# Kernel optimization log

Measured on AMD Instinct MI355X. Metric: run time of the kernel, lower is better.

Reference implementation:

```python
import jax, jax.numpy as jnp
import numpy as np

EPS = 1e-8
SCALE_FACTOR = 5.0
ITERS = 3

def _ln(x, g, b):
    m = x.mean(-1, keepdims=True)
    v = ((x - m) ** 2).mean(-1, keepdims=True)
    return (x - m) / jnp.sqrt(v + 1e-5) * g + b

def setup_inputs() -> dict:
    key = jax.random.key(0)
    ks = jax.random.split(key, 12)
    B, N, K, D = 8, 1024, 8, 256
    n01 = lambda k, s, sc=0.02: jax.random.normal(k, s, jnp.float32) * sc
    return {
        "inputs": jax.random.normal(ks[0], (B, N, D), jnp.float32),
        "conditioning": jax.random.normal(ks[1], (B, K, D + 4), jnp.float32),
        "ni_g": jnp.ones((D,), jnp.float32), "ni_b": jnp.zeros((D,), jnp.float32),
        "ns_g": jnp.ones((D,), jnp.float32), "ns_b": jnp.zeros((D,), jnp.float32),
        "wq": n01(ks[2], (D, D)), "wk": n01(ks[3], (D, D)), "wv": n01(ks[4], (D, D)),
        "gp_w": n01(ks[5], (2, D), 0.5), "gp_b": jnp.zeros((D,), jnp.float32),
        "ge_ln_g": jnp.ones((D,), jnp.float32), "ge_ln_b": jnp.zeros((D,), jnp.float32),
        "ge_w1": n01(ks[6], (D, 2 * D)), "ge_b1": jnp.zeros((2 * D,), jnp.float32),
        "ge_w2": n01(ks[7], (2 * D, D)), "ge_b2": jnp.zeros((D,), jnp.float32),
        "gru_wih": n01(ks[8], (3 * D, D)), "gru_whh": n01(ks[9], (3 * D, D)),
        "gru_bih": jnp.zeros((3 * D,), jnp.float32), "gru_bhh": jnp.zeros((3 * D,), jnp.float32),
    }

def _forward(inputs, conditioning, ni_g, ni_b, ns_g, ns_b, wq, wk, wv,
             gp_w, gp_b, ge_ln_g, ge_ln_b, ge_w1, ge_b1, ge_w2, ge_b2,
             gru_wih, gru_whh, gru_bih, gru_bhh):
    B, N, FD = inputs.shape
    D = wq.shape[1]
    attn_scale = D ** -0.5
    side = int(round(N ** 0.5))
    xs = jnp.linspace(-1.0, 1.0, side)
    abs_grid = jnp.stack(jnp.meshgrid(xs, xs, indexing="ij"), -1).reshape(N, 2)  # (N,2)

    x = _ln(inputs, ni_g, ni_b)
    k = x @ wk  # (B,N,D)
    v = x @ wv  # (B,N,D)

    def grid_enc(t):
        h = _ln(t, ge_ln_g, ge_ln_b)
        h = jax.nn.relu(h @ ge_w1 + ge_b1)
        return h @ ge_w2 + ge_b2

    def step(slots_full, update):
        slots = slots_full[..., :-4]                       # (B,K,D)
        pos = jnp.clip(slots_full[..., -4:-2], -1.0, 1.0)  # (B,K,2)
        scl = jnp.clip(slots_full[..., -2:], 1e-3, 2.0)    # (B,K,2)
        rel_grid = (abs_grid[None, None] - pos[:, :, None]) / (scl[:, :, None] * SCALE_FACTOR)  # (B,K,N,2)
        rel_enc = rel_grid @ gp_w + gp_b                   # (B,K,N,D)
        rel_k = grid_enc(k[:, None] + rel_enc)             # (B,K,N,D)
        rel_v = grid_enc(v[:, None] + rel_enc)             # (B,K,N,D)
        q = _ln(slots, ns_g, ns_b) @ wq                    # (B,K,D)
        dots = jnp.einsum("bkd,bknd->bkn", q, rel_k) * attn_scale
        attn0 = jax.nn.softmax(dots, axis=1)               # softmax over the SLOT axis
        attn = attn0 + EPS
        attn = attn / attn.sum(-1, keepdims=True)
        pos_n = jnp.einsum("bkn,nd->bkd", attn0, abs_grid)
        spread = (abs_grid[None, None] - pos_n[:, :, None]) ** 2  # (B,K,N,2)
        scl_n = jnp.clip(jnp.sqrt(jnp.einsum("bkn,bknd->bkd", attn0 + EPS, spread)), 1e-3, 2.0)
        if update:
            upd = jnp.einsum("bknd,bkn->bkd", rel_v, attn)
            gx = upd @ gru_wih.T + gru_bih
            gh = slots @ gru_whh.T + gru_bhh
            xr, xz, xn = jnp.split(gx, 3, -1)
            hr, hz, hn = jnp.split(gh, 3, -1)
            r = jax.nn.sigmoid(xr + hr)
            z = jax.nn.sigmoid(xz + hz)
            n_ = jnp.tanh(xn + r * hn)
            slots = (1.0 - z) * n_ + z * slots
        return jnp.concatenate([slots, pos_n, scl_n], -1), attn0, rel_grid

    attn0 = rel_grid = None
    for i in range(ITERS + 1):
        conditioning, attn0, rel_grid = step(conditioning, i < ITERS)
    return conditioning, attn0, rel_grid

def reference(inputs, conditioning, ni_g, ni_b, ns_g, ns_b, wq, wk, wv,
              gp_w, gp_b, ge_ln_g, ge_ln_b, ge_w1, ge_b1, ge_w2, ge_b2,
              gru_wih, gru_whh, gru_bih, gru_bhh):
    return _forward(inputs, conditioning, ni_g, ni_b, ns_g, ns_b, wq, wk, wv,
                    gp_w, gp_b, ge_ln_g, ge_ln_b, ge_w1, ge_b1, ge_w2, ge_b2,
                    gru_wih, gru_whh, gru_bih, gru_bhh)
```

## Files before the change

kernel.cpp:

```cpp
#include <hip/hip_runtime.h>
#include <math.h>

#define NB 8
#define NN 1024
#define NK 8
#define ND 256
#define ND2 512
#define NBK 64
#define EPSA 1e-8f
#define LNEPS 1e-5f
#define GSTEP (2.0f/31.0f)

using short8 = __attribute__((ext_vector_type(8))) short;
using short4v = __attribute__((ext_vector_type(4))) short;
using floatx4 = __attribute__((ext_vector_type(4))) float;

__device__ __forceinline__ short f2bf(float f) {
  unsigned u = __builtin_bit_cast(unsigned, f);
  u += 0x7fffu + ((u >> 16) & 1u);
  return (short)(u >> 16);
}
__device__ __forceinline__ float bf2f(short s) {
  unsigned u = ((unsigned)(unsigned short)s) << 16;
  return __builtin_bit_cast(float, u);
}

__global__ __launch_bounds__(256) void k_cvt_all(
    const float* __restrict__ w1, const float* __restrict__ w2,
    const float* __restrict__ wk, const float* __restrict__ wv,
    const float* __restrict__ wih, const float* __restrict__ whh,
    const float* __restrict__ wq, const float* __restrict__ b2,
    short* __restrict__ w1T, short* __restrict__ wkT, short* __restrict__ wvT,
    short* __restrict__ whhB, short* __restrict__ w2B,
    float* __restrict__ bx, float* __restrict__ vb) {
  const int idx = blockIdx.x * 256 + threadIdx.x;
  if (idx < 131072) {
    const int n = idx >> 8, k = idx & 255;
    const int dst = ((n >> 4) * 8 + (k >> 5)) * 512 + ((k >> 3) & 3) * 128 + (n & 15) * 8 + (k & 7);
    w1T[dst] = f2bf(w1[(size_t)k * 512 + n]);
  } else if (idx < 196608) {
    const int i = idx - 131072;
    const int n = i >> 8, k = i & 255;
    const int dst = ((n >> 4) * 8 + (k >> 5)) * 512 + ((k >> 3) & 3) * 128 + (n & 15) * 8 + (k & 7);
    wkT[dst] = f2bf(wk[(size_t)k * 256 + n]);
  } else if (idx < 262144) {
    const int i = idx - 196608;
    const int n = i >> 8, k = i & 255;
    const int dst = ((n >> 4) * 8 + (k >> 5)) * 512 + ((k >> 3) & 3) * 128 + (n & 15) * 8 + (k & 7);
    wvT[dst] = f2bf(wv[(size_t)k * 256 + n]);
  } else if (idx < 458752) {
    const int i = idx - 262144;
    whhB[i] = f2bf(whh[i]);
  } else if (idx < 589824) {
    const int i = idx - 458752;
    w2B[i] = f2bf(w2[i]);
  } else if (idx < 590592) {
    const int j = idx - 589824;
    float s = 0.f;
#pragma unroll 8
    for (int d = 0; d < 256; d++) s = fmaf(b2[d], wih[(size_t)j * 256 + d], s);
    bx[j] = s;
  } else if (idx < 590848) {
    const int e = idx - 590592;
    float s = 0.f;
#pragma unroll 8
    for (int d = 0; d < 256; d++) s = fmaf(wq[(size_t)e * 256 + d], b2[d], s);
    vb[e] = s;
  }
}

__global__ __launch_bounds__(256, 2) void k_mm(
    const float* __restrict__ wih, const float* __restrict__ wq,
    const short* __restrict__ w2B,
    short* __restrict__ WXT, short* __restrict__ MQ) {
  const int z = blockIdx.z;
  if (z == 1 && blockIdx.x >= 4) return;
  const float* __restrict__ A = z ? wq : wih;
  short* __restrict__ C = z ? MQ : WXT;
  __shared__ __align__(16) short As[64 * 264];
  const int row0 = blockIdx.x * 64;
  const int col0 = blockIdx.y * 128;
  const int t = threadIdx.x;
  const int wave = t >> 6, lane = t & 63, l15 = lane & 15, quad = lane >> 4;
  {
    const int r = t >> 2, sub = t & 3;
    const float* ar = A + (size_t)(row0 + r) * 256;
#pragma unroll
    for (int ii = 0; ii < 16; ii++) {
      const int d = sub * 4 + ii * 16;
      const float4 v = *(const float4*)(ar + d);
      short4v pk = {f2bf(v.x), f2bf(v.y), f2bf(v.z), f2bf(v.w)};
      *(short4v*)&As[r * 264 + d] = pk;
    }
  }
  __syncthreads();
  const short* wp = w2B + (size_t)(col0 + wave * 32 + l15) * 256 + quad * 8;
  floatx4 acc[4][2];
#pragma unroll
  for (int mt = 0; mt < 4; mt++)
#pragma unroll
    for (int nt = 0; nt < 2; nt++) acc[mt][nt] = (floatx4){0.f, 0.f, 0.f, 0.f};
#pragma unroll
  for (int kk = 0; kk < 8; kk++) {
    short8 af[4];
#pragma unroll
    for (int mt = 0; mt < 4; mt++)
      af[mt] = *(const short8*)&As[(mt * 16 + l15) * 264 + kk * 32 + quad * 8];
    short8 bf[2];
#pragma unroll
    for (int nt = 0; nt < 2; nt++)
      bf[nt] = *(const short8*)(wp + nt * 16 * 256 + kk * 32);
#pragma unroll
    for (int mt = 0; mt < 4; mt++)
#pragma unroll
      for (int nt = 0; nt < 2; nt++)
        acc[mt][nt] = __builtin_amdgcn_mfma_f32_16x16x32_bf16(af[mt], bf[nt], acc[mt][nt], 0, 0, 0);
  }
#pragma unroll
  for (int mt = 0; mt < 4; mt++)
#pragma unroll
    for (int nt = 0; nt < 2; nt++)
#pragma unroll
      for (int j = 0; j < 4; j++)
        C[(size_t)(row0 + mt * 16 + quad * 4 + j) * 512 + col0 + wave * 32 + nt * 16 + l15] =
            f2bf(acc[mt][nt][j]);
}

__global__ __launch_bounds__(256, 2) void k_gemm_kv_mfma(
    const float* __restrict__ inp,
    const float* __restrict__ nig, const float* __restrict__ nib,
    const short* __restrict__ wkT, const short* __restrict__ wvT,
    float* __restrict__ kout, float* __restrict__ vout) {
  __shared__ __align__(16) short tln[64 * 264];
  const short* __restrict__ WT = blockIdx.z ? wvT : wkT;
  float* __restrict__ out = blockIdx.z ? vout : kout;
  const int row0 = blockIdx.x * 64;
  const int t = threadIdx.x;
  const int wave = t >> 6, lane = t & 63, l15 = lane & 15, quad = lane >> 4;
  {
    const int r = t >> 2, sub = t & 3;
    const float* xr = inp + (size_t)(row0 + r) * ND;
    float tv[64];
    float sum = 0.f, ssq = 0.f;
#pragma unroll
    for (int ii = 0; ii < 16; ii++) {
      const int d = sub * 4 + ii * 16;
      const float4 xv = *(const float4*)(xr + d);
      tv[ii * 4 + 0] = xv.x; sum += xv.x; ssq += xv.x * xv.x;
      tv[ii * 4 + 1] = xv.y; sum += xv.y; ssq += xv.y * xv.y;
      tv[ii * 4 + 2] = xv.z; sum += xv.z; ssq += xv.z * xv.z;
      tv[ii * 4 + 3] = xv.w; sum += xv.w; ssq += xv.w * xv.w;
    }
    sum += __shfl_xor(sum, 1); ssq += __shfl_xor(ssq, 1);
    sum += __shfl_xor(sum, 2); ssq += __shfl_xor(ssq, 2);
    const float mean = sum * (1.0f / ND);
    const float var = ssq * (1.0f / ND) - mean * mean;
    const float rstd = rsqrtf(var + LNEPS);
#pragma unroll
    for (int ii = 0; ii < 16; ii++) {
      const int d = sub * 4 + ii * 16;
      const float4 gg = *(const float4*)(nig + d);
      const float4 bb = *(const float4*)(nib + d);
      short4v pk;
      pk.x = f2bf((tv[ii * 4 + 0] - mean) * rstd * gg.x + bb.x);
      pk.y = f2bf((tv[ii * 4 + 1] - mean) * rstd * gg.y + bb.y);
      pk.z = f2bf((tv[ii * 4 + 2] - mean) * rstd * gg.z + bb.z);
      pk.w = f2bf((tv[ii * 4 + 3] - mean) * rstd * gg.w + bb.w);
      *(short4v*)&tln[r * 264 + d] = pk;
    }
  }
  __syncthreads();
  floatx4 acc[4][4];
#pragma unroll
  for (int mt = 0; mt < 4; mt++)
#pragma unroll
    for (int nt = 0; nt < 4; nt++) acc[mt][nt] = (floatx4){0.f, 0.f, 0.f, 0.f};
  const short* wp = WT + (size_t)(wave * 32) * 512 + (size_t)lane * 8;
#pragma unroll
  for (int kk = 0; kk < 8; kk++) {
    short8 af[4];
#pragma unroll
    for (int mt = 0; mt < 4; mt++)
      af[mt] = *(const short8*)&tln[(mt * 16 + l15) * 264 + kk * 32 + quad * 8];
    short8 bf[4];
#pragma unroll
    for (int nt = 0; nt < 4; nt++)
      bf[nt] = *(const short8*)(wp + (nt * 8 + kk) * 512);
#pragma unroll
    for (int mt = 0; mt < 4; mt++)
#pragma unroll
      for (int nt = 0; nt < 4; nt++)
        acc[mt][nt] = __builtin_amdgcn_mfma_f32_16x16x32_bf16(af[mt], bf[nt], acc[mt][nt], 0, 0, 0);
  }
#pragma unroll
  for (int mt = 0; mt < 4; mt++)
#pragma unroll
    for (int nt = 0; nt < 4; nt++)
#pragma unroll
      for (int j = 0; j < 4; j++)
        out[(size_t)(row0 + mt * 16 + quad * 4 + j) * ND + wave * 64 + nt * 16 + l15] = acc[mt][nt][j];
}

__global__ __launch_bounds__(256, 2) void k_kw(
    const float* __restrict__ kbuf, const float* __restrict__ vbuf,
    const float* __restrict__ gpb, const float* __restrict__ gpw,
    const float* __restrict__ lng,
    const short* __restrict__ w1T,
    short* __restrict__ KWk, short* __restrict__ KWv,
    float* __restrict__ momk, float* __restrict__ momv) {
  __shared__ __align__(16) short tln[64 * 264];
  const float* __restrict__ src = blockIdx.z ? vbuf : kbuf;
  short* __restrict__ KW = blockIdx.z ? KWv : KWk;
  float* __restrict__ mom = blockIdx.z ? momv : momk;
  const int row0 = blockIdx.x * 64;
  const int t = threadIdx.x;
  const int wave = t >> 6, lane = t & 63, l15 = lane & 15, quad = lane >> 4;
  {
    const int r = t >> 2, sub = t & 3;
    const float* xr = src + (size_t)(row0 + r) * ND;
    float su = 0.f, sq = 0.f, sa = 0.f, sb = 0.f;
#pragma unroll
    for (int ii = 0; ii < 16; ii++) {
      const int d = sub * 4 + ii * 16;
      const float4 xv = *(const float4*)(xr + d);
      const float4 pb = *(const float4*)(gpb + d);
      const float4 wa = *(const float4*)(gpw + d);
      const float4 wb = *(const float4*)(gpw + ND + d);
      const float4 gg = *(const float4*)(lng + d);
      const float u0 = xv.x + pb.x, u1 = xv.y + pb.y, u2 = xv.z + pb.z, u3 = xv.w + pb.w;
      su += u0 + u1 + u2 + u3;
      sq += u0 * u0 + u1 * u1 + u2 * u2 + u3 * u3;
      sa += u0 * wa.x + u1 * wa.y + u2 * wa.z + u3 * wa.w;
      sb += u0 * wb.x + u1 * wb.y + u2 * wb.z + u3 * wb.w;
      short4v pk = {f2bf(u0 * gg.x), f2bf(u1 * gg.y), f2bf(u2 * gg.z), f2bf(u3 * gg.w)};
      *(short4v*)&tln[r * 264 + d] = pk;
    }
    su += __shfl_xor(su, 1); sq += __shfl_xor(sq, 1);
    sa += __shfl_xor(sa, 1); sb += __shfl_xor(sb, 1);
    su += __shfl_xor(su, 2); sq += __shfl_xor(sq, 2);
    sa += __shfl_xor(sa, 2); sb += __shfl_xor(sb, 2);
    if (sub == 0) {
      mom[(size_t)(row0 + r) * 4 + 0] = su * (1.0f / ND);
      mom[(size_t)(row0 + r) * 4 + 1] = sq * (1.0f / ND);
      mom[(size_t)(row0 + r) * 4 + 2] = sa * (1.0f / ND);
      mom[(size_t)(row0 + r) * 4 + 3] = sb * (1.0f / ND);
    }
  }
  __syncthreads();
  floatx4 acc[4][8];
#pragma unroll
  for (int mt = 0; mt < 4; mt++)
#pragma unroll
    for (int nt = 0; nt < 8; nt++) acc[mt][nt] = (floatx4){0.f, 0.f, 0.f, 0.f};
  const short* w1p = w1T + (size_t)(wave * 64) * 512 + (size_t)lane * 8;
#pragma unroll
  for (int kk = 0; kk < 8; kk++) {
    short8 af[4];
#pragma unroll
    for (int mt = 0; mt < 4; mt++)
      af[mt] = *(const short8*)&tln[(mt * 16 + l15) * 264 + kk * 32 + quad * 8];
    short8 bf[8];
#pragma unroll
    for (int nt = 0; nt < 8; nt++)
      bf[nt] = *(const short8*)(w1p + (nt * 8 + kk) * 512);
#pragma unroll
    for (int mt = 0; mt < 4; mt++)
#pragma unroll
      for (int nt = 0; nt < 8; nt++)
        acc[mt][nt] = __builtin_amdgcn_mfma_f32_16x16x32_bf16(af[mt], bf[nt], acc[mt][nt], 0, 0, 0);
  }
#pragma unroll
  for (int mt = 0; mt < 4; mt++)
#pragma unroll
    for (int nt = 0; nt < 8; nt++)
#pragma unroll
      for (int j = 0; j < 4; j++)
        KW[(size_t)(row0 + mt * 16 + quad * 4 + j) * 512 + wave * 128 + nt * 16 + l15] =
            f2bf(acc[mt][nt][j]);
}

__global__ __launch_bounds__(64) void k_vec(
    const float* __restrict__ gpw, const float* __restrict__ lng,
    const float* __restrict__ lnb, const float* __restrict__ w1,
    const float* __restrict__ b1, float* __restrict__ vecs) {
  const int v = blockIdx.x >> 3;
  const int j = (blockIdx.x & 7) * 64 + threadIdx.x;
  float s = 0.f;
#pragma unroll 4
  for (int d = 0; d < 256; d++) {
    float c;
    if (v == 0) c = gpw[d] * lng[d];
    else if (v == 1) c = gpw[256 + d] * lng[d];
    else if (v == 2) c = lng[d];
    else c = lnb[d];
    s = fmaf(c, w1[(size_t)d * 512 + j], s);
  }
  if (v == 3) s += b1[j];
  vecs[v * 512 + j] = s;
}

__global__ __launch_bounds__(256) void k_scal(const float* __restrict__ gpw,
                                              float* __restrict__ vecs) {
  const int t = threadIdx.x;
  const float wa = gpw[t], wb = gpw[256 + t];
  float v0 = wa, v1 = wb, v2 = wa * wa, v3 = wb * wb, v4 = wa * wb;
#pragma unroll
  for (int m = 32; m >= 1; m >>= 1) {
    v0 += __shfl_xor(v0, m); v1 += __shfl_xor(v1, m); v2 += __shfl_xor(v2, m);
    v3 += __shfl_xor(v3, m); v4 += __shfl_xor(v4, m);
  }
  __shared__ float red[4][5];
  if ((t & 63) == 0) {
    red[t >> 6][0] = v0; red[t >> 6][1] = v1; red[t >> 6][2] = v2;
    red[t >> 6][3] = v3; red[t >> 6][4] = v4;
  }
  __syncthreads();
  if (t < 5)
    vecs[2048 + t] = (red[0][t] + red[1][t] + red[2][t] + red[3][t]) * (1.0f / 256.0f);
}

__global__ __launch_bounds__(256) void k_dots(
    const short* __restrict__ KW, const float* __restrict__ mom,
    const float* __restrict__ vecs,
    const float* __restrict__ pos, const float* __restrict__ scl,
    const float* __restrict__ w2q, const float* __restrict__ stage,
    float* __restrict__ dots) {
  const int b = blockIdx.y, nt = blockIdx.x, kk0 = blockIdx.z * 4;
  const int t = threadIdx.x, wave = t >> 6, lane = t & 63;
  float AWv[8], BWv[8], GWv[8], bWv[8];
#pragma unroll
  for (int e = 0; e < 8; e++) {
    const int j = e * 64 + lane;
    AWv[e] = vecs[j]; BWv[e] = vecs[512 + j];
    GWv[e] = vecs[1024 + j]; bWv[e] = vecs[1536 + j];
  }
  const float mwa = vecs[2048], mwb = vecs[2049];
  const float ewa2 = vecs[2050], ewb2 = vecs[2051], ewab = vecs[2052];
  float p0[4], p1[4], si0[4], si1[4], qb2[4];
#pragma unroll
  for (int k = 0; k < 4; k++) {
    const int bk = b * 8 + kk0 + k;
    p0[k] = pos[bk * 2]; p1[k] = pos[bk * 2 + 1];
    si0[k] = 1.0f / (scl[bk * 2] * 5.0f);
    si1[k] = 1.0f / (scl[bk * 2 + 1] * 5.0f);
    qb2[k] = stage[bk * 8 + 5];
  }
#pragma unroll
  for (int i = 0; i < 2; i++) {
    const int n = nt * 8 + wave * 2 + i;
    const int row = b * NN + n;
    float KWr[8];
#pragma unroll
    for (int e = 0; e < 8; e++) KWr[e] = bf2f(KW[(size_t)row * 512 + e * 64 + lane]);
    const float mu = mom[row * 4 + 0], qm = mom[row * 4 + 1];
    const float ca = mom[row * 4 + 2], cb = mom[row * 4 + 3];
    const float gx = -1.0f + GSTEP * (float)(n >> 5);
    const float gy = -1.0f + GSTEP * (float)(n & 31);
#pragma unroll
    for (int k = 0; k < 4; k++) {
      const float rg0 = (gx - p0[k]) * si0[k];
      const float rg1 = (gy - p1[k]) * si1[k];
      const float mean = mu + rg0 * mwa + rg1 * mwb;
      const float ey2 = qm + rg0 * rg0 * ewa2 + rg1 * rg1 * ewb2 +
                        2.0f * (rg0 * ca + rg1 * cb + rg0 * rg1 * ewab);
      const float rstd = rsqrtf(ey2 - mean * mean + LNEPS);
      const float* wq = w2q + (size_t)(b * 8 + kk0 + k) * 512;
      float d = 0.f;
#pragma unroll
      for (int e = 0; e < 8; e++) {
        float tt = KWr[e];
        tt = fmaf(rg0, AWv[e], tt);
        tt = fmaf(rg1, BWv[e], tt);
        tt = fmaf(-mean, GWv[e], tt);
        const float h = fmaf(rstd, tt, bWv[e]);
        d = fmaf(fmaxf(h, 0.f), wq[e * 64 + lane], d);
      }
      d += __shfl_xor(d, 1); d += __shfl_xor(d, 2); d += __shfl_xor(d, 4);
      d += __shfl_xor(d, 8); d += __shfl_xor(d, 16); d += __shfl_xor(d, 32);
      if (lane == 0) dots[(size_t)(b * 8 + kk0 + k) * NN + n] = (d + qb2[k]) * 0.0625f;
    }
  }
}

__global__ __launch_bounds__(256) void k_ph(
    const short* __restrict__ KW, const float* __restrict__ mom,
    const float* __restrict__ vecs,
    const float* __restrict__ pos, const float* __restrict__ scl,
    const float* __restrict__ attn0, float* __restrict__ php) {
  const int b = blockIdx.y, nt = blockIdx.x, kk0 = blockIdx.z * 4;
  const int t = threadIdx.x, wave = t >> 6, lane = t & 63;
  __shared__ float phs[4 * 512];
  float AWv[8], BWv[8], GWv[8], bWv[8];
#pragma unroll
  for (int e = 0; e < 8; e++) {
    const int j = e * 64 + lane;
    AWv[e] = vecs[j]; BWv[e] = vecs[512 + j];
    GWv[e] = vecs[1024 + j]; bWv[e] = vecs[1536 + j];
  }
  const float mwa = vecs[2048], mwb = vecs[2049];
  const float ewa2 = vecs[2050], ewb2 = vecs[2051], ewab = vecs[2052];
  float p0[4], p1[4], si0[4], si1[4];
#pragma unroll
  for (int k = 0; k < 4; k++) {
    const int bk = b * 8 + kk0 + k;
    p0[k] = pos[bk * 2]; p1[k] = pos[bk * 2 + 1];
    si0[k] = 1.0f / (scl[bk * 2] * 5.0f);
    si1[k] = 1.0f / (scl[bk * 2 + 1] * 5.0f);
  }
  float acc[4][8];
#pragma unroll
  for (int k = 0; k < 4; k++)
#pragma unroll
    for (int e = 0; e < 8; e++) acc[k][e] = 0.f;
#pragma unroll
  for (int i = 0; i < 2; i++) {
    const int n = nt * 8 + wave * 2 + i;
    const int row = b * NN + n;
    float KWr[8];
#pragma unroll
    for (int e = 0; e < 8; e++) KWr[e] = bf2f(KW[(size_t)row * 512 + e * 64 + lane]);
    const float mu = mom[row * 4 + 0], qm = mom[row * 4 + 1];
    const float ca = mom[row * 4 + 2], cb = mom[row * 4 + 3];
    const float gx = -1.0f + GSTEP * (float)(n >> 5);
    const float gy = -1.0f + GSTEP * (float)(n & 31);
#pragma unroll
    for (int k = 0; k < 4; k++) {
      const float rg0 = (gx - p0[k]) * si0[k];
      const float rg1 = (gy - p1[k]) * si1[k];
      const float mean = mu + rg0 * mwa + rg1 * mwb;
      const float ey2 = qm + rg0 * rg0 * ewa2 + rg1 * rg1 * ewb2 +
                        2.0f * (rg0 * ca + rg1 * cb + rg0 * rg1 * ewab);
      const float rstd = rsqrtf(ey2 - mean * mean + LNEPS);
      const float aw = attn0[(size_t)(b * 8 + kk0 + k) * NN + n] + EPSA;
#pragma unroll
      for (int e = 0; e < 8; e++) {
        float tt = KWr[e];
        tt = fmaf(rg0, AWv[e], tt);
        tt = fmaf(rg1, BWv[e], tt);
        tt = fmaf(-mean, GWv[e], tt);
        const float h = fmaf(rstd, tt, bWv[e]);
        acc[k][e] = fmaf(aw, fmaxf(h, 0.f), acc[k][e]);
      }
    }
  }
#pragma unroll
  for (int w = 0; w < 4; w++) {
    if (wave == w) {
#pragma unroll
      for (int k = 0; k < 4; k++)
#pragma unroll
        for (int e = 0; e < 8; e++) {
          const int j = e * 64 + lane;
          if (w == 0) phs[k * 512 + j] = acc[k][e];
          else phs[k * 512 + j] += acc[k][e];
        }
    }
    __syncthreads();
  }
  float* dst = php + (size_t)(((nt * 8 + b) * 8) + kk0) * 512;
  const int base = t * 8;
  *(float4*)(dst + base) = *(const float4*)(phs + base);
  *(float4*)(dst + base + 4) = *(const float4*)(phs + base + 4);
}

__global__ __launch_bounds__(256) void k_phred(const float* __restrict__ php,
                                               const float* __restrict__ stage,
                                               float* __restrict__ ph) {
  const int bk = blockIdx.x, t = threadIdx.x;
  const int b = bk >> 3, k = bk & 7;
  const float dn = 1.0f / (stage[bk * 8 + 0] + (float)NN * EPSA);
  float s0 = 0.f, s1 = 0.f;
#pragma unroll 4
  for (int p = 0; p < 128; p++) {
    const float* src = php + (size_t)((p * 8 + b) * 8 + k) * 512;
    s0 += src[t];
    s1 += src[t + 256];
  }
  ph[bk * 512 + t] = s0 * dn;
  ph[bk * 512 + 256 + t] = s1 * dn;
}

__global__ __launch_bounds__(64) void k_softmax_reduce(
    const float* __restrict__ dots, float* __restrict__ attn0,
    float* __restrict__ stage) {
  const int t = threadIdx.x;
  const int idx = blockIdx.x * 64 + t;
  const int b = idx >> 10, n = idx & 1023;
  float vals[NK];
  float mx = -1e30f;
#pragma unroll
  for (int k = 0; k < NK; k++) {
    vals[k] = dots[(size_t)(b * NK + k) * NN + n];
    mx = fmaxf(mx, vals[k]);
  }
  float s = 0.f;
#pragma unroll
  for (int k = 0; k < NK; k++) { vals[k] = expf(vals[k] - mx); s += vals[k]; }
  const float inv = 1.0f / s;
  const float gx = -1.0f + GSTEP * (float)(n >> 5);
  const float gy = -1.0f + GSTEP * (float)(n & 31);
  const float gx2 = gx * gx, gy2 = gy * gy;
  float sk[NK][5];
#pragma unroll
  for (int k = 0; k < NK; k++) {
    const float a = vals[k] * inv;
    attn0[(size_t)(b * NK + k) * NN + n] = a;
    const float w = a + EPSA;
    sk[k][0] = a;
    sk[k][1] = a * gx;
    sk[k][2] = a * gy;
    sk[k][3] = w * gx2;
    sk[k][4] = w * gy2;
  }
#pragma unroll
  for (int m = 32; m >= 1; m >>= 1)
#pragma unroll
    for (int k = 0; k < NK; k++)
#pragma unroll
      for (int c = 0; c < 5; c++)
        sk[k][c] += __shfl_xor(sk[k][c], m);
  __shared__ float red[40];
  if (t == 0) {
#pragma unroll
    for (int k = 0; k < NK; k++)
#pragma unroll
      for (int c = 0; c < 5; c++)
        red[k * 5 + c] = sk[k][c];
  }
  __syncthreads();
  if (t < 40) {
    const int k = t / 5, c = t % 5;
    atomicAdd(&stage[(b * NK + k) * 8 + c], red[t]);
  }
}

__global__ __launch_bounds__(256) void k_gatesC(
    const float* __restrict__ ph, const float* __restrict__ sf,
    const short* __restrict__ WXT, const short* __restrict__ whhB,
    const float* __restrict__ bx, short* __restrict__ gxh) {
  __shared__ __align__(16) short A[64 * 264];
  const int c = blockIdx.x;
  const int isX = (c < 6) ? 1 : 0;
  const int jb = (isX ? c : c - 6) * 128;
  const int t = threadIdx.x;
  const int wave = t >> 6, lane = t & 63, l15 = lane & 15, quad = lane >> 4;
  const int r = t >> 2, sub = t & 3;
  floatx4 acc[4][2];
#pragma unroll
  for (int mt = 0; mt < 4; mt++)
#pragma unroll
    for (int nt = 0; nt < 2; nt++) acc[mt][nt] = (floatx4){0.f, 0.f, 0.f, 0.f};

  if (isX) {
#pragma unroll
    for (int half = 0; half < 2; half++) {
      if (half > 0) __syncthreads();
#pragma unroll
      for (int ii = 0; ii < 16; ii++) {
        const int d = sub * 4 + ii * 16;
        const float4 v = *(const float4*)(ph + r * 512 + half * 256 + d);
        short4v pk = {f2bf(v.x), f2bf(v.y), f2bf(v.z), f2bf(v.w)};
        *(short4v*)&A[r * 264 + d] = pk;
      }
      __syncthreads();
      const short* wp = WXT + (size_t)(jb + wave * 32 + l15) * 512 + half * 256 + quad * 8;
#pragma unroll
      for (int kk = 0; kk < 8; kk++) {
        short8 af[4];
#pragma unroll
        for (int mt = 0; mt < 4; mt++)
          af[mt] = *(const short8*)&A[(mt * 16 + l15) * 264 + kk * 32 + quad * 8];
        short8 bf[2];
#pragma unroll
        for (int nt = 0; nt < 2; nt++)
          bf[nt] = *(const short8*)(wp + nt * 16 * 512 + kk * 32);
#pragma unroll
        for (int mt = 0; mt < 4; mt++)
#pragma unroll
          for (int nt = 0; nt < 2; nt++)
            acc[mt][nt] = __builtin_amdgcn_mfma_f32_16x16x32_bf16(af[mt], bf[nt], acc[mt][nt], 0, 0, 0);
      }
    }
#pragma unroll
    for (int nt = 0; nt < 2; nt++) {
      const int col = jb + wave * 32 + nt * 16 + l15;
      const float bxv = bx[col];
#pragma unroll
      for (int mt = 0; mt < 4; mt++)
#pragma unroll
        for (int j = 0; j < 4; j++)
          gxh[(mt * 16 + quad * 4 + j) * 1536 + col] = f2bf(acc[mt][nt][j] + bxv);
    }
  } else {
#pragma unroll
    for (int ii = 0; ii < 16; ii++) {
      const int d = sub * 4 + ii * 16;
      const float4 v = *(const float4*)(sf + r * 260 + d);
      short4v pk = {f2bf(v.x), f2bf(v.y), f2bf(v.z), f2bf(v.w)};
      *(short4v*)&A[r * 264 + d] = pk;
    }
    __syncthreads();
    const short* wp = whhB + (size_t)(jb + wave * 32 + l15) * 256 + quad * 8;
#pragma unroll
    for (int kk = 0; kk < 8; kk++) {
      short8 af[4];
#pragma unroll
      for (int mt = 0; mt < 4; mt++)
        af[mt] = *(const short8*)&A[(mt * 16 + l15) * 264 + kk * 32 + quad * 8];
      short8 bf[2];
#pragma unroll
      for (int nt = 0; nt < 2; nt++)
        bf[nt] = *(const short8*)(wp + nt * 16 * 256 + kk * 32);
#pragma unroll
      for (int mt = 0; mt < 4; mt++)
#pragma unroll
        for (int nt = 0; nt < 2; nt++)
          acc[mt][nt] = __builtin_amdgcn_mfma_f32_16x16x32_bf16(af[mt], bf[nt], acc[mt][nt], 0, 0, 0);
    }
#pragma unroll
    for (int mt = 0; mt < 4; mt++)
#pragma unroll
      for (int nt = 0; nt < 2; nt++)
#pragma unroll
        for (int j = 0; j < 4; j++)
          gxh[(mt * 16 + quad * 4 + j) * 1536 + 768 + jb + wave * 32 + nt * 16 + l15] =
              f2bf(acc[mt][nt][j]);
    }
}

__global__ __launch_bounds__(256) void k_slotW(
    const short* __restrict__ gxh, float* __restrict__ sf,
    const float* __restrict__ cond,
    const float* __restrict__ bih, const float* __restrict__ bhh,
    const float* __restrict__ nsg, const float* __restrict__ nsb,
    const short* __restrict__ MQ, const float* __restrict__ vb,
    float* __restrict__ w2q, float* __restrict__ pos, float* __restrict__ scl,
    float* __restrict__ stage, const int mode) {
  const int bk = blockIdx.x, t = threadIdx.x;
  __shared__ float lnvS[256];
  __shared__ float red[8];
  const int wv = t >> 6;
  float ns;
  if (mode) {
    const float h = sf[bk * 260 + t];
    const float x0 = bf2f(gxh[bk * 1536 + t]);
    const float x1 = bf2f(gxh[bk * 1536 + 256 + t]);
    const float x2 = bf2f(gxh[bk * 1536 + 512 + t]);
    const float h0 = bf2f(gxh[bk * 1536 + 768 + t]);
    const float h1v = bf2f(gxh[bk * 1536 + 1024 + t]);
    const float h2 = bf2f(gxh[bk * 1536 + 1280 + t]);
    const float r = 1.0f / (1.0f + expf(-(x0 + bih[t] + h0 + bhh[t])));
    const float z = 1.0f / (1.0f + expf(-(x1 + bih[256 + t] + h1v + bhh[256 + t])));
    const float nw = tanhf(x2 + bih[512 + t] + r * (h2 + bhh[512 + t]));
    ns = (1.0f - z) * nw + z * h;
    sf[bk * 260 + t] = ns;
  } else {
    ns = cond[bk * 260 + t];
    sf[bk * 260 + t] = ns;
    if (t < 4) sf[bk * 260 + 256 + t] = cond[bk * 260 + 256 + t];
  }
  float s2 = ns, ss = ns * ns;
#pragma unroll
  for (int m = 32; m >= 1; m >>= 1) { s2 += __shfl_xor(s2, m); ss += __shfl_xor(ss, m); }
  if ((t & 63) == 0) { red[wv] = s2; red[4 + wv] = ss; }
  __syncthreads();
  const float S = red[0] + red[1] + red[2] + red[3];
  const float SS = red[4] + red[5] + red[6] + red[7];
  const float mean = S * (1.0f / ND);
  const float var = SS * (1.0f / ND) - mean * mean;
  const float rstd = rsqrtf(var + LNEPS);
  const float lnv = (ns - mean) * rstd * nsg[t] + nsb[t];
  lnvS[t] = lnv;
  if (mode) {
    if (t == 0) {
      const float Sa = stage[bk * 8 + 0];
      const float G0 = stage[bk * 8 + 1];
      const float G1 = stage[bk * 8 + 2];
      const float Q0 = stage[bk * 8 + 3];
      const float Q1 = stage[bk * 8 + 4];
      const float W = Sa + (float)NN * EPSA;
      const float sc0 = sqrtf(fmaxf(Q0 - 2.0f * G0 * G0 + G0 * G0 * W, 0.f));
      const float sc1 = sqrtf(fmaxf(Q1 - 2.0f * G1 * G1 + G1 * G1 * W, 0.f));
      const float sc0c = fminf(fmaxf(sc0, 1e-3f), 2.0f);
      const float sc1c = fminf(fmaxf(sc1, 1e-3f), 2.0f);
      sf[bk * 260 + 256] = G0;
      sf[bk * 260 + 257] = G1;
      sf[bk * 260 + 258] = sc0c;
      sf[bk * 260 + 259] = sc1c;
      pos[bk * 2 + 0] = fminf(fmaxf(G0, -1.0f), 1.0f);
      pos[bk * 2 + 1] = fminf(fmaxf(G1, -1.0f), 1.0f);
      scl[bk * 2 + 0] = sc0c;
      scl[bk * 2 + 1] = sc1c;
    }
  } else {
    if (t < 2) {
      const float p = cond[bk * 260 + 256 + t];
      pos[bk * 2 + t] = fminf(fmaxf(p, -1.0f), 1.0f);
      const float sc = cond[bk * 260 + 258 + t];
      scl[bk * 2 + t] = fminf(fmaxf(sc, 1e-3f), 2.0f);
    }
  }
  __syncthreads();
  if (t < 5) stage[bk * 8 + t] = 0.f;
  float w0 = 0.f, w1v = 0.f;
#pragma unroll 8
  for (int e = 0; e < ND; e++) {
    const float lv = lnvS[e];
    w0 = fmaf(lv, bf2f(MQ[e * 512 + t]), w0);
    w1v = fmaf(lv, bf2f(MQ[e * 512 + 256 + t]), w1v);
  }
  w2q[bk * 512 + t] = w0;
  w2q[bk * 512 + 256 + t] = w1v;
  float qd = lnvS[t] * vb[t];
#pragma unroll
  for (int m = 32; m >= 1; m >>= 1) qd += __shfl_xor(qd, m);
  __syncthreads();
  if ((t & 63) == 0) red[wv] = qd;
  __syncthreads();
  if (t == 0) stage[bk * 8 + 5] = red[0] + red[1] + red[2] + red[3];
}

__global__ __launch_bounds__(256) void k_finalize(
    const float* __restrict__ sf, const float* __restrict__ attn0,
    const float* __restrict__ pos, const float* __restrict__ scl,
    const float* __restrict__ stage, float* __restrict__ out) {
  const int bk = blockIdx.x, t = threadIdx.x;
  out[bk * 260 + t] = sf[bk * 260 + t];
  if (t == 0) {
    const float Sa = stage[bk * 8 + 0];
    const float G0 = stage[bk * 8 + 1];
    const float G1 = stage[bk * 8 + 2];
    const float Q0 = stage[bk * 8 + 3];
    const float Q1 = stage[bk * 8 + 4];
    const float W = Sa + (float)NN * EPSA;
    const float sc0 = sqrtf(fmaxf(Q0 - 2.0f * G0 * G0 + G0 * G0 * W, 0.f));
    const float sc1 = sqrtf(fmaxf(Q1 - 2.0f * G1 * G1 + G1 * G1 * W, 0.f));
    out[bk * 260 + 256] = G0;
    out[bk * 260 + 257] = G1;
    out[bk * 260 + 258] = fminf(fmaxf(sc0, 1e-3f), 2.0f);
    out[bk * 260 + 259] = fminf(fmaxf(sc1, 1e-3f), 2.0f);
  }
  const float p0 = pos[bk * 2 + 0], p1 = pos[bk * 2 + 1];
  const float s0 = scl[bk * 2 + 0] * 5.0f, s1 = scl[bk * 2 + 1] * 5.0f;
#pragma unroll
  for (int i = 0; i < 4; i++) {
    const int n = t + 256 * i;
    out[16640 + bk * NN + n] = attn0[(size_t)bk * NN + n];
    const float gx = -1.0f + GSTEP * (float)(n >> 5);
    const float gy = -1.0f + GSTEP * (float)(n & 31);
    float2 v;
    v.x = (gx - p0) / s0;
    v.y = (gy - p1) / s1;
    *(float2*)(out + 16640 + 65536 + ((size_t)bk * NN + n) * 2) = v;
  }
}

extern "C" void kernel_launch(void* const* d_in, const int* in_sizes, int n_in,
                              void* d_out, int out_size, void* d_ws, size_t ws_size,
                              hipStream_t stream) {
  const float* inputs   = (const float*)d_in[0];
  const float* cond     = (const float*)d_in[1];
  const float* ni_g     = (const float*)d_in[2];
  const float* ni_b     = (const float*)d_in[3];
  const float* ns_g     = (const float*)d_in[4];
  const float* ns_b     = (const float*)d_in[5];
  const float* wq       = (const float*)d_in[6];
  const float* wk       = (const float*)d_in[7];
  const float* wv       = (const float*)d_in[8];
  const float* gp_w     = (const float*)d_in[9];
  const float* gp_b     = (const float*)d_in[10];
  const float* ge_ln_g  = (const float*)d_in[11];
  const float* ge_ln_b  = (const float*)d_in[12];
  const float* ge_w1    = (const float*)d_in[13];
  const float* ge_b1    = (const float*)d_in[14];
  const float* ge_w2    = (const float*)d_in[15];
  const float* ge_b2    = (const float*)d_in[16];
  const float* gru_wih  = (const float*)d_in[17];
  const float* gru_whh  = (const float*)d_in[18];
  const float* gru_bih  = (const float*)d_in[19];
  const float* gru_bhh  = (const float*)d_in[20];

  float* ws   = (float*)d_ws;
  float* kbuf = ws;
  float* vbuf = kbuf + 2097152;
  float* php  = ws;
  float* sf   = vbuf + 2097152;
  float* w2qb = sf + 16640;
  float* posb = w2qb + 32768;
  float* sclb = posb + 128;
  float* dotsb = sclb + 128;
  float* at0  = dotsb + 65536;
  float* phb  = at0 + 65536;
  float* stag = phb + 32768;
  float* bxb  = stag + 512;
  float* vbb  = bxb + 768;
  float* momk = vbb + 256;
  float* momv = momk + 32768;
  float* vecs = momv + 32768;
  float* unused_php = vecs + 2560;
  short* gxh  = (short*)(unused_php + 2097152);
  short* w1T  = gxh + 98304;
  short* wkT  = w1T + 131072;
  short* wvT  = wkT + 65536;
  short* whhB = wvT + 65536;
  short* w2B  = whhB + 196608;
  short* WXT  = w2B + 131072;
  short* MQ   = WXT + 393216;
  short* KWk  = MQ + 131072;
  short* KWv  = KWk + 4194304;

  float* out = (float*)d_out;

  k_cvt_all<<<2308, 256, 0, stream>>>(ge_w1, ge_w2, wk, wv, gru_wih, gru_whh, wq,
                                      ge_b2, w1T, wkT, wvT, whhB, w2B, bxb, vbb);
  k_mm<<<dim3(12, 4, 2), 256, 0, stream>>>(gru_wih, wq, w2B, WXT, MQ);
  k_gemm_kv_mfma<<<dim3(128, 1, 2), 256, 0, stream>>>(inputs, ni_g, ni_b,
                                                      wkT, wvT, kbuf, vbuf);
  k_vec<<<32, 64, 0, stream>>>(gp_w, ge_ln_g, ge_ln_b, ge_w1, ge_b1, vecs);
  k_scal<<<1, 256, 0, stream>>>(gp_w, vecs);
  k_kw<<<dim3(128, 1, 2), 256, 0, stream>>>(kbuf, vbuf, gp_b, gp_w, ge_ln_g,
                                            w1T, KWk, KWv, momk, momv);
  k_slotW<<<NBK, 256, 0, stream>>>(gxh, sf, cond, gru_bih, gru_bhh, ns_g, ns_b,
                                   MQ, vbb, w2qb, posb, sclb, stag, 0);

  for (int s = 0; s < 4; s++) {
    k_dots<<<dim3(128, NB, 2), 256, 0, stream>>>(KWk, momk, vecs, posb, sclb,
                                                 w2qb, stag, dotsb);
    k_softmax_reduce<<<128, 64, 0, stream>>>(dotsb, at0, stag);
    if (s < 3) {
      k_ph<<<dim3(128, NB, 2), 256, 0, stream>>>(KWv, momv, vecs, posb, sclb,
                                                 at0, php);
      k_phred<<<NBK, 256, 0, stream>>>(php, stag, phb);
      k_gatesC<<<12, 256, 0, stream>>>(phb, sf, WXT, whhB, bxb, gxh);
      k_slotW<<<NBK, 256, 0, stream>>>(gxh, sf, cond, gru_bih, gru_bhh, ns_g, ns_b,
                                       MQ, vbb, w2qb, posb, sclb, stag, 1);
    }
  }

  k_finalize<<<NBK, 256, 0, stream>>>(sf, at0, posb, sclb, stag, out);
}
```

Measured before the change: 443.3 us.

## Fuse KV projection with KW GEMM, merge GRU tail kernels, fold setup kernels

Fuses the K/V projection GEMM with the following w1 GEMM and moment computation, so the fp32 K/V intermediates never go through global memory. Folds the k_vec and k_scal setup kernels into the weight conversion kernel. Replaces the phred, gatesC and slotW kernels in each iteration with one per-slot k_tail kernel that uses transposed weights for coalesced GEMV access, and halves the k_ph grid so each block covers more rows. This removes launches and intermediate traffic, but the GRU GEMMs now run as scalar GEMVs over only 64 blocks instead of MFMA tiles.

```diff
diff --git a/kernel.cpp b/kernel.cpp
--- a/kernel.cpp
+++ b/kernel.cpp
@@ -30,9 +30,11 @@
     const float* __restrict__ wk, const float* __restrict__ wv,
     const float* __restrict__ wih, const float* __restrict__ whh,
     const float* __restrict__ wq, const float* __restrict__ b2,
+    const float* __restrict__ gpw, const float* __restrict__ lng,
+    const float* __restrict__ lnb, const float* __restrict__ b1,
     short* __restrict__ w1T, short* __restrict__ wkT, short* __restrict__ wvT,
-    short* __restrict__ whhB, short* __restrict__ w2B,
-    float* __restrict__ bx, float* __restrict__ vb) {
+    short* __restrict__ whhBt, short* __restrict__ w2B,
+    float* __restrict__ bx, float* __restrict__ vb, float* __restrict__ vecs) {
   const int idx = blockIdx.x * 256 + threadIdx.x;
   if (idx < 131072) {
     const int n = idx >> 8, k = idx & 255;
@@ -50,7 +52,8 @@
     wvT[dst] = f2bf(wv[(size_t)k * 256 + n]);
   } else if (idx < 458752) {
     const int i = idx - 262144;
-    whhB[i] = f2bf(whh[i]);
+    const int j = i >> 8, d = i & 255;
+    whhBt[(size_t)d * 768 + j] = f2bf(whh[i]);
   } else if (idx < 589824) {
     const int i = idx - 458752;
     w2B[i] = f2bf(w2[i]);
@@ -66,17 +69,46 @@
 #pragma unroll 8
     for (int d = 0; d < 256; d++) s = fmaf(wq[(size_t)e * 256 + d], b2[d], s);
     vb[e] = s;
+  } else if (idx < 592896) {
+    const int vi = idx - 590848;
+    const int v = vi >> 9, j = vi & 511;
+    float s = 0.f;
+#pragma unroll 4
+    for (int d = 0; d < 256; d++) {
+      float c;
+      if (v == 0) c = gpw[d] * lng[d];
+      else if (v == 1) c = gpw[256 + d] * lng[d];
+      else if (v == 2) c = lng[d];
+      else c = lnb[d];
+      s = fmaf(c, w1[(size_t)d * 512 + j], s);
+    }
+    if (v == 3) s += b1[j];
+    vecs[v * 512 + j] = s;
+  } else if (idx < 592901) {
+    const int sc = idx - 592896;
+    float s = 0.f;
+#pragma unroll 4
+    for (int d = 0; d < 256; d++) {
+      const float wa = gpw[d], wb = gpw[256 + d];
+      float c;
+      if (sc == 0) c = wa;
+      else if (sc == 1) c = wb;
+      else if (sc == 2) c = wa * wa;
+      else if (sc == 3) c = wb * wb;
+      else c = wa * wb;
+      s += c;
+    }
+    vecs[2048 + sc] = s * (1.0f / 256.0f);
   }
 }
 
 __global__ __launch_bounds__(256, 2) void k_mm(
     const float* __restrict__ wih, const float* __restrict__ wq,
     const short* __restrict__ w2B,
-    short* __restrict__ WXT, short* __restrict__ MQ) {
+    short* __restrict__ WXTt, short* __restrict__ MQ) {
   const int z = blockIdx.z;
   if (z == 1 && blockIdx.x >= 4) return;
   const float* __restrict__ A = z ? wq : wih;
-  short* __restrict__ C = z ? MQ : WXT;
   __shared__ __align__(16) short As[64 * 264];
   const int row0 = blockIdx.x * 64;
   const int col0 = blockIdx.y * 128;
@@ -121,19 +153,29 @@
 #pragma unroll
     for (int nt = 0; nt < 2; nt++)
 #pragma unroll
-      for (int j = 0; j < 4; j++)
-        C[(size_t)(row0 + mt * 16 + quad * 4 + j) * 512 + col0 + wave * 32 + nt * 16 + l15] =
-            f2bf(acc[mt][nt][j]);
-}
-
-__global__ __launch_bounds__(256, 2) void k_gemm_kv_mfma(
+      for (int j = 0; j < 4; j++) {
+        const int row = row0 + mt * 16 + quad * 4 + j;
+        const int col = col0 + wave * 32 + nt * 16 + l15;
+        const short val = f2bf(acc[mt][nt][j]);
+        if (z) MQ[(size_t)row * 512 + col] = val;
+        else WXTt[(size_t)col * 768 + row] = val;
+      }
+}
+
+__global__ __launch_bounds__(256, 2) void k_kv_kw(
     const float* __restrict__ inp,
     const float* __restrict__ nig, const float* __restrict__ nib,
     const short* __restrict__ wkT, const short* __restrict__ wvT,
-    float* __restrict__ kout, float* __restrict__ vout) {
+    const float* __restrict__ gpb, const float* __restrict__ gpw,
+    const float* __restrict__ lng,
+    const short* __restrict__ w1T,
+    short* __restrict__ KWk, short* __restrict__ KWv,
+    float* __restrict__ momk, float* __restrict__ momv) {
   __shared__ __align__(16) short tln[64 * 264];
+  __shared__ float momS[64][4][4];
   const short* __restrict__ WT = blockIdx.z ? wvT : wkT;
-  float* __restrict__ out = blockIdx.z ? vout : kout;
+  short* __restrict__ KW = blockIdx.z ? KWv : KWk;
+  float* __restrict__ mom = blockIdx.z ? momv : momk;
   const int row0 = blockIdx.x * 64;
   const int t = threadIdx.x;
   const int wave = t >> 6, lane = t & 63, l15 = lane & 15, quad = lane >> 4;
@@ -175,83 +217,75 @@
   for (int mt = 0; mt < 4; mt++)
 #pragma unroll
     for (int nt = 0; nt < 4; nt++) acc[mt][nt] = (floatx4){0.f, 0.f, 0.f, 0.f};
-  const short* wp = WT + (size_t)(wave * 32) * 512 + (size_t)lane * 8;
-#pragma unroll
-  for (int kk = 0; kk < 8; kk++) {
-    short8 af[4];
+  {
+    const short* wp = WT + (size_t)(wave * 32) * 512 + (size_t)lane * 8;
+#pragma unroll
+    for (int kk = 0; kk < 8; kk++) {
+      short8 af[4];
+#pragma unroll
+      for (int mt = 0; mt < 4; mt++)
+        af[mt] = *(const short8*)&tln[(mt * 16 + l15) * 264 + kk * 32 + quad * 8];
+      short8 bf[4];
+#pragma unroll
+      for (int nt = 0; nt < 4; nt++)
+        bf[nt] = *(const short8*)(wp + (nt * 8 + kk) * 512);
+#pragma unroll
+      for (int mt = 0; mt < 4; mt++)
+#pragma unroll
+        for (int nt = 0; nt < 4; nt++)
+          acc[mt][nt] = __builtin_amdgcn_mfma_f32_16x16x32_bf16(af[mt], bf[nt], acc[mt][nt], 0, 0, 0);
+    }
+  }
+  __syncthreads();
+  {
+    float waL[4], wbL[4], ggL[4], pbL[4];
+#pragma unroll
+    for (int nt = 0; nt < 4; nt++) {
+      const int c = wave * 64 + nt * 16 + l15;
+      waL[nt] = gpw[c]; wbL[nt] = gpw[256 + c];
+      ggL[nt] = lng[c]; pbL[nt] = gpb[c];
+    }
 #pragma unroll
     for (int mt = 0; mt < 4; mt++)
-      af[mt] = *(const short8*)&tln[(mt * 16 + l15) * 264 + kk * 32 + quad * 8];
-    short8 bf[4];
-#pragma unroll
-    for (int nt = 0; nt < 4; nt++)
-      bf[nt] = *(const short8*)(wp + (nt * 8 + kk) * 512);
-#pragma unroll
-    for (int mt = 0; mt < 4; mt++)
-#pragma unroll
-      for (int nt = 0; nt < 4; nt++)
-        acc[mt][nt] = __builtin_amdgcn_mfma_f32_16x16x32_bf16(af[mt], bf[nt], acc[mt][nt], 0, 0, 0);
-  }
+#pragma unroll
+      for (int j = 0; j < 4; j++) {
+        const int row = mt * 16 + quad * 4 + j;
+        float su = 0.f, sq = 0.f, sa = 0.f, sb = 0.f;
+#pragma unroll
+        for (int nt = 0; nt < 4; nt++) {
+          const float u = acc[mt][nt][j] + pbL[nt];
+          su += u; sq += u * u; sa += u * waL[nt]; sb += u * wbL[nt];
+          tln[row * 264 + wave * 64 + nt * 16 + l15] = f2bf(u * ggL[nt]);
+        }
+        su += __shfl_xor(su, 1); sq += __shfl_xor(sq, 1);
+        sa += __shfl_xor(sa, 1); sb += __shfl_xor(sb, 1);
+        su += __shfl_xor(su, 2); sq += __shfl_xor(sq, 2);
+        sa += __shfl_xor(sa, 2); sb += __shfl_xor(sb, 2);
+        su += __shfl_xor(su, 4); sq += __shfl_xor(sq, 4);
+        sa += __shfl_xor(sa, 4); sb += __shfl_xor(sb, 4);
+        su += __shfl_xor(su, 8); sq += __shfl_xor(sq, 8);
+        sa += __shfl_xor(sa, 8); sb += __shfl_xor(sb, 8);
+        if (l15 == 0) {
+          momS[row][wave][0] = su; momS[row][wave][1] = sq;
+          momS[row][wave][2] = sa; momS[row][wave][3] = sb;
+        }
+      }
+  }
+  __syncthreads();
+  if (t < 64) {
+    const float m0 = momS[t][0][0] + momS[t][1][0] + momS[t][2][0] + momS[t][3][0];
+    const float m1 = momS[t][0][1] + momS[t][1][1] + momS[t][2][1] + momS[t][3][1];
+    const float m2 = momS[t][0][2] + momS[t][1][2] + momS[t][2][2] + momS[t][3][2];
+    const float m3 = momS[t][0][3] + momS[t][1][3] + momS[t][2][3] + momS[t][3][3];
+    float* mp = mom + (size_t)(row0 + t) * 4;
+    mp[0] = m0 * (1.0f / ND); mp[1] = m1 * (1.0f / ND);
+    mp[2] = m2 * (1.0f / ND); mp[3] = m3 * (1.0f / ND);
+  }
+  floatx4 acc2[4][8];
 #pragma unroll
   for (int mt = 0; mt < 4; mt++)
 #pragma unroll
-    for (int nt = 0; nt < 4; nt++)
-#pragma unroll
-      for (int j = 0; j < 4; j++)
-        out[(size_t)(row0 + mt * 16 + quad * 4 + j) * ND + wave * 64 + nt * 16 + l15] = acc[mt][nt][j];
-}
-
-__global__ __launch_bounds__(256, 2) void k_kw(
-    const float* __restrict__ kbuf, const float* __restrict__ vbuf,
-    const float* __restrict__ gpb, const float* __restrict__ gpw,
-    const float* __restrict__ lng,
-    const short* __restrict__ w1T,
-    short* __restrict__ KWk, short* __restrict__ KWv,
-    float* __restrict__ momk, float* __restrict__ momv) {
-  __shared__ __align__(16) short tln[64 * 264];
-  const float* __restrict__ src = blockIdx.z ? vbuf : kbuf;
-  short* __restrict__ KW = blockIdx.z ? KWv : KWk;
-  float* __restrict__ mom = blockIdx.z ? momv : momk;
-  const int row0 = blockIdx.x * 64;
-  const int t = threadIdx.x;
-  const int wave = t >> 6, lane = t & 63, l15 = lane & 15, quad = lane >> 4;
-  {
-    const int r = t >> 2, sub = t & 3;
-    const float* xr = src + (size_t)(row0 + r) * ND;
-    float su = 0.f, sq = 0.f, sa = 0.f, sb = 0.f;
-#pragma unroll
-    for (int ii = 0; ii < 16; ii++) {
-      const int d = sub * 4 + ii * 16;
-      const float4 xv = *(const float4*)(xr + d);
-      const float4 pb = *(const float4*)(gpb + d);
-      const float4 wa = *(const float4*)(gpw + d);
-      const float4 wb = *(const float4*)(gpw + ND + d);
-      const float4 gg = *(const float4*)(lng + d);
-      const float u0 = xv.x + pb.x, u1 = xv.y + pb.y, u2 = xv.z + pb.z, u3 = xv.w + pb.w;
-      su += u0 + u1 + u2 + u3;
-      sq += u0 * u0 + u1 * u1 + u2 * u2 + u3 * u3;
-      sa += u0 * wa.x + u1 * wa.y + u2 * wa.z + u3 * wa.w;
-      sb += u0 * wb.x + u1 * wb.y + u2 * wb.z + u3 * wb.w;
-      short4v pk = {f2bf(u0 * gg.x), f2bf(u1 * gg.y), f2bf(u2 * gg.z), f2bf(u3 * gg.w)};
-      *(short4v*)&tln[r * 264 + d] = pk;
-    }
-    su += __shfl_xor(su, 1); sq += __shfl_xor(sq, 1);
-    sa += __shfl_xor(sa, 1); sb += __shfl_xor(sb, 1);
-    su += __shfl_xor(su, 2); sq += __shfl_xor(sq, 2);
-    sa += __shfl_xor(sa, 2); sb += __shfl_xor(sb, 2);
-    if (sub == 0) {
-      mom[(size_t)(row0 + r) * 4 + 0] = su * (1.0f / ND);
-      mom[(size_t)(row0 + r) * 4 + 1] = sq * (1.0f / ND);
-      mom[(size_t)(row0 + r) * 4 + 2] = sa * (1.0f / ND);
-      mom[(size_t)(row0 + r) * 4 + 3] = sb * (1.0f / ND);
-    }
-  }
-  __syncthreads();
-  floatx4 acc[4][8];
-#pragma unroll
-  for (int mt = 0; mt < 4; mt++)
-#pragma unroll
-    for (int nt = 0; nt < 8; nt++) acc[mt][nt] = (floatx4){0.f, 0.f, 0.f, 0.f};
+    for (int nt = 0; nt < 8; nt++) acc2[mt][nt] = (floatx4){0.f, 0.f, 0.f, 0.f};
   const short* w1p = w1T + (size_t)(wave * 64) * 512 + (size_t)lane * 8;
 #pragma unroll
   for (int kk = 0; kk < 8; kk++) {
@@ -267,7 +301,7 @@
     for (int mt = 0; mt < 4; mt++)
 #pragma unroll
       for (int nt = 0; nt < 8; nt++)
-        acc[mt][nt] = __builtin_amdgcn_mfma_f32_16x16x32_bf16(af[mt], bf[nt], acc[mt][nt], 0, 0, 0);
+        acc2[mt][nt] = __builtin_amdgcn_mfma_f32_16x16x32_bf16(af[mt], bf[nt], acc2[mt][nt], 0, 0, 0);
   }
 #pragma unroll
   for (int mt = 0; mt < 4; mt++)
@@ -276,47 +310,7 @@
 #pragma unroll
       for (int j = 0; j < 4; j++)
         KW[(size_t)(row0 + mt * 16 + quad * 4 + j) * 512 + wave * 128 + nt * 16 + l15] =
-            f2bf(acc[mt][nt][j]);
-}
-
-__global__ __launch_bounds__(64) void k_vec(
-    const float* __restrict__ gpw, const float* __restrict__ lng,
-    const float* __restrict__ lnb, const float* __restrict__ w1,
-    const float* __restrict__ b1, float* __restrict__ vecs) {
-  const int v = blockIdx.x >> 3;
-  const int j = (blockIdx.x & 7) * 64 + threadIdx.x;
-  float s = 0.f;
-#pragma unroll 4
-  for (int d = 0; d < 256; d++) {
-    float c;
-    if (v == 0) c = gpw[d] * lng[d];
-    else if (v == 1) c = gpw[256 + d] * lng[d];
-    else if (v == 2) c = lng[d];
-    else c = lnb[d];
-    s = fmaf(c, w1[(size_t)d * 512 + j], s);
-  }
-  if (v == 3) s += b1[j];
-  vecs[v * 512 + j] = s;
-}
-
-__global__ __launch_bounds__(256) void k_scal(const float* __restrict__ gpw,
-                                              float* __restrict__ vecs) {
-  const int t = threadIdx.x;
-  const float wa = gpw[t], wb = gpw[256 + t];
-  float v0 = wa, v1 = wb, v2 = wa * wa, v3 = wb * wb, v4 = wa * wb;
-#pragma unroll
-  for (int m = 32; m >= 1; m >>= 1) {
-    v0 += __shfl_xor(v0, m); v1 += __shfl_xor(v1, m); v2 += __shfl_xor(v2, m);
-    v3 += __shfl_xor(v3, m); v4 += __shfl_xor(v4, m);
-  }
-  __shared__ float red[4][5];
-  if ((t & 63) == 0) {
-    red[t >> 6][0] = v0; red[t >> 6][1] = v1; red[t >> 6][2] = v2;
-    red[t >> 6][3] = v3; red[t >> 6][4] = v4;
-  }
-  __syncthreads();
-  if (t < 5)
-    vecs[2048 + t] = (red[0][t] + red[1][t] + red[2][t] + red[3][t]) * (1.0f / 256.0f);
+            f2bf(acc2[mt][nt][j]);
 }
 
 __global__ __launch_bounds__(256) void k_dots(
@@ -413,8 +407,8 @@
 #pragma unroll
     for (int e = 0; e < 8; e++) acc[k][e] = 0.f;
 #pragma unroll
-  for (int i = 0; i < 2; i++) {
-    const int n = nt * 8 + wave * 2 + i;
+  for (int i = 0; i < 4; i++) {
+    const int n = nt * 16 + wave * 4 + i;
     const int row = b * NN + n;
     float KWr[8];
 #pragma unroll
@@ -461,23 +455,6 @@
   const int base = t * 8;
   *(float4*)(dst + base) = *(const float4*)(phs + base);
   *(float4*)(dst + base + 4) = *(const float4*)(phs + base + 4);
-}
-
-__global__ __launch_bounds__(256) void k_phred(const float* __restrict__ php,
-                                               const float* __restrict__ stage,
-                                               float* __restrict__ ph) {
-  const int bk = blockIdx.x, t = threadIdx.x;
-  const int b = bk >> 3, k = bk & 7;
-  const float dn = 1.0f / (stage[bk * 8 + 0] + (float)NN * EPSA);
-  float s0 = 0.f, s1 = 0.f;
-#pragma unroll 4
-  for (int p = 0; p < 128; p++) {
-    const float* src = php + (size_t)((p * 8 + b) * 8 + k) * 512;
-    s0 += src[t];
-    s1 += src[t + 256];
-  }
-  ph[bk * 512 + t] = s0 * dn;
-  ph[bk * 512 + 256 + t] = s1 * dn;
 }
 
 __global__ __launch_bounds__(64) void k_softmax_reduce(
@@ -534,131 +511,57 @@
   }
 }
 
-__global__ __launch_bounds__(256) void k_gatesC(
-    const float* __restrict__ ph, const float* __restrict__ sf,
-    const short* __restrict__ WXT, const short* __restrict__ whhB,
-    const float* __restrict__ bx, short* __restrict__ gxh) {
-  __shared__ __align__(16) short A[64 * 264];
-  const int c = blockIdx.x;
-  const int isX = (c < 6) ? 1 : 0;
-  const int jb = (isX ? c : c - 6) * 128;
-  const int t = threadIdx.x;
-  const int wave = t >> 6, lane = t & 63, l15 = lane & 15, quad = lane >> 4;
-  const int r = t >> 2, sub = t & 3;
-  floatx4 acc[4][2];
-#pragma unroll
-  for (int mt = 0; mt < 4; mt++)
-#pragma unroll
-    for (int nt = 0; nt < 2; nt++) acc[mt][nt] = (floatx4){0.f, 0.f, 0.f, 0.f};
-
-  if (isX) {
-#pragma unroll
-    for (int half = 0; half < 2; half++) {
-      if (half > 0) __syncthreads();
-#pragma unroll
-      for (int ii = 0; ii < 16; ii++) {
-        const int d = sub * 4 + ii * 16;
-        const float4 v = *(const float4*)(ph + r * 512 + half * 256 + d);
-        short4v pk = {f2bf(v.x), f2bf(v.y), f2bf(v.z), f2bf(v.w)};
-        *(short4v*)&A[r * 264 + d] = pk;
-      }
-      __syncthreads();
-      const short* wp = WXT + (size_t)(jb + wave * 32 + l15) * 512 + half * 256 + quad * 8;
-#pragma unroll
-      for (int kk = 0; kk < 8; kk++) {
-        short8 af[4];
-#pragma unroll
-        for (int mt = 0; mt < 4; mt++)
-          af[mt] = *(const short8*)&A[(mt * 16 + l15) * 264 + kk * 32 + quad * 8];
-        short8 bf[2];
-#pragma unroll
-        for (int nt = 0; nt < 2; nt++)
-          bf[nt] = *(const short8*)(wp + nt * 16 * 512 + kk * 32);
-#pragma unroll
-        for (int mt = 0; mt < 4; mt++)
-#pragma unroll
-          for (int nt = 0; nt < 2; nt++)
-            acc[mt][nt] = __builtin_amdgcn_mfma_f32_16x16x32_bf16(af[mt], bf[nt], acc[mt][nt], 0, 0, 0);
-      }
-    }
-#pragma unroll
-    for (int nt = 0; nt < 2; nt++) {
-      const int col = jb + wave * 32 + nt * 16 + l15;
-      const float bxv = bx[col];
-#pragma unroll
-      for (int mt = 0; mt < 4; mt++)
-#pragma unroll
-        for (int j = 0; j < 4; j++)
-          gxh[(mt * 16 + quad * 4 + j) * 1536 + col] = f2bf(acc[mt][nt][j] + bxv);
-    }
-  } else {
-#pragma unroll
-    for (int ii = 0; ii < 16; ii++) {
-      const int d = sub * 4 + ii * 16;
-      const float4 v = *(const float4*)(sf + r * 260 + d);
-      short4v pk = {f2bf(v.x), f2bf(v.y), f2bf(v.z), f2bf(v.w)};
-      *(short4v*)&A[r * 264 + d] = pk;
-    }
-    __syncthreads();
-    const short* wp = whhB + (size_t)(jb + wave * 32 + l15) * 256 + quad * 8;
-#pragma unroll
-    for (int kk = 0; kk < 8; kk++) {
-      short8 af[4];
-#pragma unroll
-      for (int mt = 0; mt < 4; mt++)
-        af[mt] = *(const short8*)&A[(mt * 16 + l15) * 264 + kk * 32 + quad * 8];
-      short8 bf[2];
-#pragma unroll
-      for (int nt = 0; nt < 2; nt++)
-        bf[nt] = *(const short8*)(wp + nt * 16 * 256 + kk * 32);
-#pragma unroll
-      for (int mt = 0; mt < 4; mt++)
-#pragma unroll
-        for (int nt = 0; nt < 2; nt++)
-          acc[mt][nt] = __builtin_amdgcn_mfma_f32_16x16x32_bf16(af[mt], bf[nt], acc[mt][nt], 0, 0, 0);
-    }
-#pragma unroll
-    for (int mt = 0; mt < 4; mt++)
-#pragma unroll
-      for (int nt = 0; nt < 2; nt++)
-#pragma unroll
-        for (int j = 0; j < 4; j++)
-          gxh[(mt * 16 + quad * 4 + j) * 1536 + 768 + jb + wave * 32 + nt * 16 + l15] =
-              f2bf(acc[mt][nt][j]);
-    }
-}
-
-__global__ __launch_bounds__(256) void k_slotW(
-    const short* __restrict__ gxh, float* __restrict__ sf,
-    const float* __restrict__ cond,
+__global__ __launch_bounds__(256) void k_tail(
+    const float* __restrict__ php, float* __restrict__ sf,
+    const short* __restrict__ WXTt, const short* __restrict__ whhBt,
+    const float* __restrict__ bx,
     const float* __restrict__ bih, const float* __restrict__ bhh,
     const float* __restrict__ nsg, const float* __restrict__ nsb,
     const short* __restrict__ MQ, const float* __restrict__ vb,
     float* __restrict__ w2q, float* __restrict__ pos, float* __restrict__ scl,
-    float* __restrict__ stage, const int mode) {
+    float* __restrict__ stage) {
   const int bk = blockIdx.x, t = threadIdx.x;
+  const int b = bk >> 3, k = bk & 7;
+  __shared__ float phv[512];
+  __shared__ float sfv[256];
   __shared__ float lnvS[256];
   __shared__ float red[8];
   const int wv = t >> 6;
-  float ns;
-  if (mode) {
-    const float h = sf[bk * 260 + t];
-    const float x0 = bf2f(gxh[bk * 1536 + t]);
-    const float x1 = bf2f(gxh[bk * 1536 + 256 + t]);
-    const float x2 = bf2f(gxh[bk * 1536 + 512 + t]);
-    const float h0 = bf2f(gxh[bk * 1536 + 768 + t]);
-    const float h1v = bf2f(gxh[bk * 1536 + 1024 + t]);
-    const float h2 = bf2f(gxh[bk * 1536 + 1280 + t]);
-    const float r = 1.0f / (1.0f + expf(-(x0 + bih[t] + h0 + bhh[t])));
-    const float z = 1.0f / (1.0f + expf(-(x1 + bih[256 + t] + h1v + bhh[256 + t])));
-    const float nw = tanhf(x2 + bih[512 + t] + r * (h2 + bhh[512 + t]));
-    ns = (1.0f - z) * nw + z * h;
-    sf[bk * 260 + t] = ns;
-  } else {
-    ns = cond[bk * 260 + t];
-    sf[bk * 260 + t] = ns;
-    if (t < 4) sf[bk * 260 + 256 + t] = cond[bk * 260 + 256 + t];
-  }
+  sfv[t] = sf[bk * 260 + t];
+  const float dn = 1.0f / (stage[bk * 8 + 0] + (float)NN * EPSA);
+  float s0 = 0.f, s1 = 0.f;
+#pragma unroll 4
+  for (int p = 0; p < 64; p++) {
+    const float* src = php + (size_t)((p * 8 + b) * 8 + k) * 512;
+    s0 += src[t];
+    s1 += src[t + 256];
+  }
+  phv[t] = s0 * dn;
+  phv[t + 256] = s1 * dn;
+  __syncthreads();
+  float x0 = bx[t], x1 = bx[256 + t], x2 = bx[512 + t];
+#pragma unroll 8
+  for (int e = 0; e < 512; e++) {
+    const float pv = phv[e];
+    const short* wrow = WXTt + (size_t)e * 768;
+    x0 = fmaf(pv, bf2f(wrow[t]), x0);
+    x1 = fmaf(pv, bf2f(wrow[256 + t]), x1);
+    x2 = fmaf(pv, bf2f(wrow[512 + t]), x2);
+  }
+  float h0 = 0.f, h1v = 0.f, h2 = 0.f;
+#pragma unroll 8
+  for (int d = 0; d < 256; d++) {
+    const float sv = sfv[d];
+    const short* hrow = whhBt + (size_t)d * 768;
+    h0 = fmaf(sv, bf2f(hrow[t]), h0);
+    h1v = fmaf(sv, bf2f(hrow[256 + t]), h1v);
+    h2 = fmaf(sv, bf2f(hrow[512 + t]), h2);
+  }
+  const float r = 1.0f / (1.0f + expf(-(x0 + bih[t] + h0 + bhh[t])));
+  const float z = 1.0f / (1.0f + expf(-(x1 + bih[256 + t] + h1v + bhh[256 + t])));
+  const float nw = tanhf(x2 + bih[512 + t] + r * (h2 + bhh[512 + t]));
+  const float ns = (1.0f - z) * nw + z * sfv[t];
+  sf[bk * 260 + t] = ns;
   float s2 = ns, ss = ns * ns;
 #pragma unroll
   for (int m = 32; m >= 1; m >>= 1) { s2 += __shfl_xor(s2, m); ss += __shfl_xor(ss, m); }
@@ -671,34 +574,76 @@
   const float rstd = rsqrtf(var + LNEPS);
   const float lnv = (ns - mean) * rstd * nsg[t] + nsb[t];
   lnvS[t] = lnv;
-  if (mode) {
-    if (t == 0) {
-      const float Sa = stage[bk * 8 + 0];
-      const float G0 = stage[bk * 8 + 1];
-      const float G1 = stage[bk * 8 + 2];
-      const float Q0 = stage[bk * 8 + 3];
-      const float Q1 = stage[bk * 8 + 4];
-      const float W = Sa + (float)NN * EPSA;
-      const float sc0 = sqrtf(fmaxf(Q0 - 2.0f * G0 * G0 + G0 * G0 * W, 0.f));
-      const float sc1 = sqrtf(fmaxf(Q1 - 2.0f * G1 * G1 + G1 * G1 * W, 0.f));
-      const float sc0c = fminf(fmaxf(sc0, 1e-3f), 2.0f);
-      const float sc1c = fminf(fmaxf(sc1, 1e-3f), 2.0f);
-      sf[bk * 260 + 256] = G0;
-      sf[bk * 260 + 257] = G1;
-      sf[bk * 260 + 258] = sc0c;
-      sf[bk * 260 + 259] = sc1c;
-      pos[bk * 2 + 0] = fminf(fmaxf(G0, -1.0f), 1.0f);
-      pos[bk * 2 + 1] = fminf(fmaxf(G1, -1.0f), 1.0f);
-      scl[bk * 2 + 0] = sc0c;
-      scl[bk * 2 + 1] = sc1c;
-    }
-  } else {
-    if (t < 2) {
-      const float p = cond[bk * 260 + 256 + t];
-      pos[bk * 2 + t] = fminf(fmaxf(p, -1.0f), 1.0f);
-      const float sc = cond[bk * 260 + 258 + t];
-      scl[bk * 2 + t] = fminf(fmaxf(sc, 1e-3f), 2.0f);
-    }
+  if (t == 0) {
+    const float Sa = stage[bk * 8 + 0];
+    const float G0 = stage[bk * 8 + 1];
+    const float G1 = stage[bk * 8 + 2];
+    const float Q0 = stage[bk * 8 + 3];
+    const float Q1 = stage[bk * 8 + 4];
+    const float W = Sa + (float)NN * EPSA;
+    const float sc0 = sqrtf(fmaxf(Q0 - 2.0f * G0 * G0 + G0 * G0 * W, 0.f));
+    const float sc1 = sqrtf(fmaxf(Q1 - 2.0f * G1 * G1 + G1 * G1 * W, 0.f));
+    const float sc0c = fminf(fmaxf(sc0, 1e-3f), 2.0f);
+    const float sc1c = fminf(fmaxf(sc1, 1e-3f), 2.0f);
+    sf[bk * 260 + 256] = G0;
+    sf[bk * 260 + 257] = G1;
+    sf[bk * 260 + 258] = sc0c;
+    sf[bk * 260 + 259] = sc1c;
+    pos[bk * 2 + 0] = fminf(fmaxf(G0, -1.0f), 1.0f);
+    pos[bk * 2 + 1] = fminf(fmaxf(G1, -1.0f), 1.0f);
+    scl[bk * 2 + 0] = sc0c;
+    scl[bk * 2 + 1] = sc1c;
+  }
+  __syncthreads();
+  if (t < 5) stage[bk * 8 + t] = 0.f;
+  float w0 = 0.f, w1v = 0.f;
+#pragma unroll 8
+  for (int e = 0; e < ND; e++) {
+    const float lv = lnvS[e];
+    w0 = fmaf(lv, bf2f(MQ[e * 512 + t]), w0);
+    w1v = fmaf(lv, bf2f(MQ[e * 512 + 256 + t]), w1v);
+  }
+  w2q[bk * 512 + t] = w0;
+  w2q[bk * 512 + 256 + t] = w1v;
+  float qd = lnvS[t] * vb[t];
+#pragma unroll
+  for (int m = 32; m >= 1; m >>= 1) qd += __shfl_xor(qd, m);
+  __syncthreads();
+  if ((t & 63) == 0) red[wv] = qd;
+  __syncthreads();
+  if (t == 0) stage[bk * 8 + 5] = red[0] + red[1] + red[2] + red[3];
+}
+
+__global__ __launch_bounds__(256) void k_slot0(
+    float* __restrict__ sf, const float* __restrict__ cond,
+    const float* __restrict__ nsg, const float* __restrict__ nsb,
+    const short* __restrict__ MQ, const float* __restrict__ vb,
+    float* __restrict__ w2q, float* __restrict__ pos, float* __restrict__ scl,
+    float* __restrict__ stage) {
+  const int bk = blockIdx.x, t = threadIdx.x;
+  __shared__ float lnvS[256];
+  __shared__ float red[8];
+  const int wv = t >> 6;
+  const float ns = cond[bk * 260 + t];
+  sf[bk * 260 + t] = ns;
+  if (t < 4) sf[bk * 260 + 256 + t] = cond[bk * 260 + 256 + t];
+  float s2 = ns, ss = ns * ns;
+#pragma unroll
+  for (int m = 32; m >= 1; m >>= 1) { s2 += __shfl_xor(s2, m); ss += __shfl_xor(ss, m); }
+  if ((t & 63) == 0) { red[wv] = s2; red[4 + wv] = ss; }
+  __syncthreads();
+  const float S = red[0] + red[1] + red[2] + red[3];
+  const float SS = red[4] + red[5] + red[6] + red[7];
+  const float mean = S * (1.0f / ND);
+  const float var = SS * (1.0f / ND) - mean * mean;
+  const float rstd = rsqrtf(var + LNEPS);
+  const float lnv = (ns - mean) * rstd * nsg[t] + nsb[t];
+  lnvS[t] = lnv;
+  if (t < 2) {
+    const float p = cond[bk * 260 + 256 + t];
+    pos[bk * 2 + t] = fminf(fmaxf(p, -1.0f), 1.0f);
+    const float sc = cond[bk * 260 + 258 + t];
+    scl[bk * 2 + t] = fminf(fmaxf(sc, 1e-3f), 2.0f);
   }
   __syncthreads();
   if (t < 5) stage[bk * 8 + t] = 0.f;
@@ -781,59 +726,51 @@
   const float* gru_bhh  = (const float*)d_in[20];
 
   float* ws   = (float*)d_ws;
-  float* kbuf = ws;
-  float* vbuf = kbuf + 2097152;
   float* php  = ws;
-  float* sf   = vbuf + 2097152;
+  float* sf   = php + 2097152;
   float* w2qb = sf + 16640;
   float* posb = w2qb + 32768;
   float* sclb = posb + 128;
   float* dotsb = sclb + 128;
   float* at0  = dotsb + 65536;
-  float* phb  = at0 + 65536;
-  float* stag = phb + 32768;
+  float* stag = at0 + 65536;
   float* bxb  = stag + 512;
   float* vbb  = bxb + 768;
   float* momk = vbb + 256;
   float* momv = momk + 32768;
   float* vecs = momv + 32768;
-  float* unused_php = vecs + 2560;
-  short* gxh  = (short*)(unused_php + 2097152);
-  short* w1T  = gxh + 98304;
+  short* w1T  = (short*)(vecs + 2560);
   short* wkT  = w1T + 131072;
   short* wvT  = wkT + 65536;
-  short* whhB = wvT + 65536;
-  short* w2B  = whhB + 196608;
-  short* WXT  = w2B + 131072;
-  short* MQ   = WXT + 393216;
+  short* whhBt = wvT + 65536;
+  short* w2B  = whhBt + 196608;
+  short* WXTt = w2B + 131072;
+  short* MQ   = WXTt + 393216;
   short* KWk  = MQ + 131072;
   short* KWv  = KWk + 4194304;
 
   float* out = (float*)d_out;
 
-  k_cvt_all<<<2308, 256, 0, stream>>>(ge_w1, ge_w2, wk, wv, gru_wih, gru_whh, wq,
-                                      ge_b2, w1T, wkT, wvT, whhB, w2B, bxb, vbb);
-  k_mm<<<dim3(12, 4, 2), 256, 0, stream>>>(gru_wih, wq, w2B, WXT, MQ);
-  k_gemm_kv_mfma<<<dim3(128, 1, 2), 256, 0, stream>>>(inputs, ni_g, ni_b,
-                                                      wkT, wvT, kbuf, vbuf);
-  k_vec<<<32, 64, 0, stream>>>(gp_w, ge_ln_g, ge_ln_b, ge_w1, ge_b1, vecs);
-  k_scal<<<1, 256, 0, stream>>>(gp_w, vecs);
-  k_kw<<<dim3(128, 1, 2), 256, 0, stream>>>(kbuf, vbuf, gp_b, gp_w, ge_ln_g,
-                                            w1T, KWk, KWv, momk, momv);
-  k_slotW<<<NBK, 256, 0, stream>>>(gxh, sf, cond, gru_bih, gru_bhh, ns_g, ns_b,
-                                   MQ, vbb, w2qb, posb, sclb, stag, 0);
+  k_cvt_all<<<2317, 256, 0, stream>>>(ge_w1, ge_w2, wk, wv, gru_wih, gru_whh, wq,
+                                      ge_b2, gp_w, ge_ln_g, ge_ln_b, ge_b1,
+                                      w1T, wkT, wvT, whhBt, w2B, bxb, vbb, vecs);
+  k_mm<<<dim3(12, 4, 2), 256, 0, stream>>>(gru_wih, wq, w2B, WXTt, MQ);
+  k_kv_kw<<<dim3(128, 1, 2), 256, 0, stream>>>(inputs, ni_g, ni_b, wkT, wvT,
+                                               gp_b, gp_w, ge_ln_g, w1T,
+                                               KWk, KWv, momk, momv);
+  k_slot0<<<NBK, 256, 0, stream>>>(sf, cond, ns_g, ns_b, MQ, vbb,
+                                   w2qb, posb, sclb, stag);
 
   for (int s = 0; s < 4; s++) {
     k_dots<<<dim3(128, NB, 2), 256, 0, stream>>>(KWk, momk, vecs, posb, sclb,
                                                  w2qb, stag, dotsb);
     k_softmax_reduce<<<128, 64, 0, stream>>>(dotsb, at0, stag);
     if (s < 3) {
-      k_ph<<<dim3(128, NB, 2), 256, 0, stream>>>(KWv, momv, vecs, posb, sclb,
-                                                 at0, php);
-      k_phred<<<NBK, 256, 0, stream>>>(php, stag, phb);
-      k_gatesC<<<12, 256, 0, stream>>>(phb, sf, WXT, whhB, bxb, gxh);
-      k_slotW<<<NBK, 256, 0, stream>>>(gxh, sf, cond, gru_bih, gru_bhh, ns_g, ns_b,
-                                       MQ, vbb, w2qb, posb, sclb, stag, 1);
+      k_ph<<<dim3(64, NB, 2), 256, 0, stream>>>(KWv, momv, vecs, posb, sclb,
+                                                at0, php);
+      k_tail<<<NBK, 256, 0, stream>>>(php, sf, WXTt, whhBt, bxb,
+                                      gru_bih, gru_bhh, ns_g, ns_b, MQ, vbb,
+                                      w2qb, posb, sclb, stag);
     }
   }
 
```

Result: slower. 480.2 us (+8.3%).
